# Kernel tuning notes

Measured on AMD Instinct MI355X. Metric: run time of the kernel, lower is better.

Reference implementation:

```python
import jax, jax.numpy as jnp
import numpy as np

N, E, D, L, G = 100000, 300000, 256, 5, 4096


def _bn(x, p):
    # p: [4, dim] = (gamma, beta, running_mean, running_var); eval-mode BatchNorm1d
    g, b, m, v = p
    return (x - m) * jax.lax.rsqrt(v + 1e-5) * g + b


def setup_inputs() -> dict:
    key = jax.random.key(0)
    ks = iter(jax.random.split(key, 48))

    def nrm(shape, scale=0.02):
        return jax.random.normal(next(ks), shape, dtype=jnp.float32) * scale

    def bn_params(n, dim):
        g = 1.0 + nrm((n, dim), 0.1)
        b = nrm((n, dim), 0.1)
        m = nrm((n, dim), 0.1)
        v = 1.0 + jax.random.uniform(next(ks), (n, dim), dtype=jnp.float32)
        return jnp.stack([g, b, m, v], axis=1)  # [n,4,dim]

    return {
        "x": jax.random.randint(next(ks), (N, 9), 0, 2, dtype=jnp.int32),
        "edge_index": jax.random.randint(next(ks), (2, E), 0, N, dtype=jnp.int32),
        "edge_attr": jax.random.randint(next(ks), (E, 3), 0, 2, dtype=jnp.int32),
        "batch": jnp.sort(jax.random.randint(next(ks), (N,), 0, G, dtype=jnp.int32)),
        "atom_emb": nrm((9, 120, D)),            # AtomEncoder: 9 feature tables
        "bond_emb": nrm((L, 3, 6, D)),           # per-layer BondEncoder: 3 feature tables
        "vn0": jnp.zeros((D,), jnp.float32),     # virtualnode embedding (init 0)
        "eps": jnp.zeros((L,), jnp.float32),     # GIN eps per layer
        "conv_W1": nrm((L, D, 2 * D), 1.0 / np.sqrt(D)),     # GIN MLP (sampled BayesLinear)
        "conv_b1": nrm((L, 2 * D)),
        "conv_bn1": bn_params(L, 2 * D),
        "conv_W2": nrm((L, 2 * D, D), 1.0 / np.sqrt(2 * D)),
        "conv_b2": nrm((L, D)),
        "node_bn": bn_params(L, D),              # per-layer outer BatchNorm
        "vn_W1": nrm((L - 1, D, D), 1.0 / np.sqrt(D)),       # virtual-node MLP
        "vn_b1": nrm((L - 1, D)),
        "vn_bn1": bn_params(L - 1, D),
        "vn_W2": nrm((L - 1, D, D), 1.0 / np.sqrt(D)),
        "vn_b2": nrm((L - 1, D)),
        "vn_bn2": bn_params(L - 1, D),
    }


def reference(x, edge_index, edge_attr, batch, atom_emb, bond_emb, vn0, eps,
              conv_W1, conv_b1, conv_bn1, conv_W2, conv_b2, node_bn,
              vn_W1, vn_b1, vn_bn1, vn_W2, vn_b2, vn_bn2):
    src, dst = edge_index[0], edge_index[1]
    n_nodes = x.shape[0]
    n_layers = conv_W1.shape[0]
    # AtomEncoder: sum of 9 feature embeddings -> [N, D]
    h = atom_emb[jnp.arange(9), x].sum(axis=1)
    vn = jnp.broadcast_to(vn0, (G, vn0.shape[0]))  # [G, D]
    for l in range(n_layers):
        # broadcast virtual node into graph's nodes
        h = h + vn[batch]
        # GINConv: msg = relu(x_j + bond_emb), sum-aggregate, MLP((1+eps)x + aggr)
        e = bond_emb[l][jnp.arange(3), edge_attr].sum(axis=1)  # [E, D]
        msg = jax.nn.relu(h[src] + e)
        aggr = jax.ops.segment_sum(msg, dst, num_segments=n_nodes)
        t = (1.0 + eps[l]) * h + aggr
        t = jax.nn.relu(_bn(t @ conv_W1[l] + conv_b1[l], conv_bn1[l])) @ conv_W2[l] + conv_b2[l]
        hn = _bn(t, node_bn[l])  # outer BatchNorm (eval); dropout is identity in eval
        if l < n_layers - 1:
            hn = jax.nn.relu(hn)
            # global_add_pool of pre-conv h, then virtual-node MLP update
            vtemp = jax.ops.segment_sum(h, batch, num_segments=G) + vn
            u = jax.nn.relu(_bn(vtemp @ vn_W1[l] + vn_b1[l], vn_bn1[l]))
            vn = jax.nn.relu(_bn(u @ vn_W2[l] + vn_b2[l], vn_bn2[l]))
        h = hn
    return h  # JK == 'last'
```

## Files before the change

kernel.cpp:

```cpp
#include <hip/hip_runtime.h>

#define NN 100000
#define EE 300000
#define DD 256
#define LL 5
#define GG 4096
#define DB 512
#define MPAD 100096

typedef __attribute__((ext_vector_type(4))) float f32x4;
typedef __attribute__((ext_vector_type(8))) short s16x8;

__device__ __forceinline__ ushort f2bf(float f) {
  unsigned u = __float_as_uint(f);
  return (ushort)((u + 0x7fffu + ((u >> 16) & 1u)) >> 16);
}
__device__ __forceinline__ float b2f(ushort u) {
  return __uint_as_float(((unsigned)u) << 16);
}

__device__ __forceinline__ void gload16(const void* g, void* l) {
  __builtin_amdgcn_global_load_lds((const __attribute__((address_space(1))) void*)g,
                                   (__attribute__((address_space(3))) void*)l, 16, 0, 0);
}

__global__ void k_atom(const int* __restrict__ x, const float* __restrict__ emb,
                       const float* __restrict__ vn0, ushort* __restrict__ hvb) {
  int n = blockIdx.x * 4 + (threadIdx.x >> 6);
  if (n >= NN) return;
  int d = (threadIdx.x & 63) * 4;
  const float4 v0 = *(const float4*)&vn0[d];
  float ax = v0.x, ay = v0.y, az = v0.z, aw = v0.w;
#pragma unroll
  for (int f = 0; f < 9; ++f) {
    int v = x[n * 9 + f];
    const float4 t = *(const float4*)&emb[((size_t)(f * 120 + v)) * DD + d];
    ax += t.x; ay += t.y; az += t.z; aw += t.w;
  }
  ushort4 o; o.x = f2bf(ax); o.y = f2bf(ay); o.z = f2bf(az); o.w = f2bf(aw);
  *(ushort4*)&hvb[(size_t)n * DD + d] = o;
}

__global__ void k_vninit(const float* __restrict__ vn0, float* __restrict__ vn) {
  int i = blockIdx.x * blockDim.x + threadIdx.x;
  if (i < GG * DD) vn[i] = vn0[i & (DD - 1)];
}

__global__ void k_goff(const int* __restrict__ batch, int* __restrict__ goff) {
  int g = blockIdx.x * blockDim.x + threadIdx.x;
  if (g > GG) return;
  if (g == GG) { goff[GG] = NN; return; }
  int lo = 0, hi = NN;
  while (lo < hi) { int mid = (lo + hi) >> 1; if (batch[mid] < g) lo = mid + 1; else hi = mid; }
  goff[g] = lo;
}

__global__ void k_zero(int* __restrict__ p, int n) {
  int i = blockIdx.x * 256 + threadIdx.x;
  if (i < n) p[i] = 0;
}

__global__ void k_deg(const int* __restrict__ dst, int* __restrict__ deg) {
  int e = blockIdx.x * 256 + threadIdx.x;
  if (e < EE) atomicAdd(&deg[dst[e]], 1);
}

__global__ void k_scan1(const int* __restrict__ deg, int* __restrict__ coff,
                        int* __restrict__ bsum) {
  __shared__ int wsum[16];
  __shared__ int wpre[16];
  int lane = threadIdx.x & 63, wid = threadIdx.x >> 6;
  int i = blockIdx.x * 1024 + threadIdx.x;
  int v = (i < NN) ? deg[i] : 0;
  int xv = v;
#pragma unroll
  for (int off = 1; off < 64; off <<= 1) {
    int y = __shfl_up(xv, off);
    if (lane >= off) xv += y;
  }
  if (lane == 63) wsum[wid] = xv;
  __syncthreads();
  if (wid == 0 && lane < 16) {
    int s = wsum[lane];
    int xx = s;
#pragma unroll
    for (int off = 1; off < 16; off <<= 1) {
      int y = __shfl_up(xx, off);
      if (lane >= off) xx += y;
    }
    wpre[lane] = xx - s;
  }
  __syncthreads();
  int val = xv + wpre[wid];
  if (i < NN) coff[i + 1] = val;
  if (threadIdx.x == 1023) bsum[blockIdx.x] = val;
}

__global__ void k_scan2(int* __restrict__ bsum, int nb) {
  __shared__ int ws[2];
  int t = threadIdx.x, lane = t & 63, wid = t >> 6;
  int v = (t < nb) ? bsum[t] : 0;
  int xv = v;
#pragma unroll
  for (int off = 1; off < 64; off <<= 1) {
    int y = __shfl_up(xv, off);
    if (lane >= off) xv += y;
  }
  if (lane == 63) ws[wid] = xv;
  __syncthreads();
  int incl = xv + ((wid == 1) ? ws[0] : 0);
  if (t < nb) bsum[t] = incl - v;
}

__global__ void k_scan3(int* __restrict__ coff, const int* __restrict__ bpre) {
  int i = blockIdx.x * 1024 + threadIdx.x;
  if (i == 0) coff[0] = 0;
  if (i < NN) coff[i + 1] += bpre[i >> 10];
}

__global__ void k_eposinit(const int* __restrict__ coff, int* __restrict__ epos) {
  int n = blockIdx.x * 256 + threadIdx.x;
  if (n < NN) epos[n] = coff[n];
}

__global__ void k_scatter(const int* __restrict__ dst, int* __restrict__ epos,
                          int* __restrict__ eid) {
  int e = blockIdx.x * 256 + threadIdx.x;
  if (e < EE) { int p = atomicAdd(&epos[dst[e]], 1); eid[p] = e; }
}

__global__ void k_sort(const int* __restrict__ coff, int* __restrict__ eid) {
  int n = blockIdx.x * 256 + threadIdx.x;
  if (n >= NN) return;
  int s = coff[n], t = coff[n + 1];
  for (int i = s + 1; i < t; ++i) {
    int key = eid[i]; int j = i - 1;
    while (j >= s && eid[j] > key) { eid[j + 1] = eid[j]; --j; }
    eid[j + 1] = key;
  }
}

__global__ void k_emeta(const int* __restrict__ eid, const int* __restrict__ srcs,
                        const int* __restrict__ eattr, unsigned* __restrict__ emeta) {
  int idx = blockIdx.x * 256 + threadIdx.x;
  if (idx >= EE) return;
  int e = eid[idx];
  int s = srcs[e];
  unsigned c = (unsigned)(eattr[e * 3 + 0] + 2 * eattr[e * 3 + 1] + 4 * eattr[e * 3 + 2]);
  emeta[idx] = (unsigned)s | (c << 17);
}

__global__ void k_bond8(const float* __restrict__ bondE, float* __restrict__ bond8) {
  int l = blockIdx.x, c = blockIdx.y, d = threadIdx.x;
  float v = bondE[(((size_t)l * 3 + 0) * 6 + (c & 1)) * DD + d]
          + bondE[(((size_t)l * 3 + 1) * 6 + ((c >> 1) & 1)) * DD + d]
          + bondE[(((size_t)l * 3 + 2) * 6 + ((c >> 2) & 1)) * DD + d];
  bond8[((size_t)l * 8 + c) * DD + d] = v;
}

__global__ void k_wt(const float* __restrict__ in, ushort* __restrict__ out, int K, int N) {
  __shared__ float t[16][17];
  int l = blockIdx.z;
  int kb = blockIdx.x * 16, nb = blockIdx.y * 16;
  int tx = threadIdx.x & 15, ty = threadIdx.x >> 4;
  t[ty][tx] = in[(size_t)l * K * N + (size_t)(kb + ty) * N + nb + tx];
  __syncthreads();
  out[(size_t)l * N * K + (size_t)(nb + ty) * K + kb + tx] = f2bf(t[tx][ty]);
}

__global__ void k_pool(const ushort* __restrict__ hvb, const float* __restrict__ vn,
                       ushort* __restrict__ vtempb, const int* __restrict__ goff) {
  int g = blockIdx.x * 4 + (threadIdx.x >> 6);
  if (g >= GG) return;
  int d = (threadIdx.x & 63) * 4;
  float4 v = *(const float4*)&vn[(size_t)g * DD + d];
  float ax = v.x, ay = v.y, az = v.z, aw = v.w;
  int r0 = goff[g], r1 = goff[g + 1];
  for (int r = r0; r < r1; ++r) {
    ushort4 hu = *(const ushort4*)&hvb[(size_t)r * DD + d];
    ax += b2f(hu.x); ay += b2f(hu.y); az += b2f(hu.z); aw += b2f(hu.w);
  }
  ushort4 o; o.x = f2bf(ax); o.y = f2bf(ay); o.z = f2bf(az); o.w = f2bf(aw);
  *(ushort4*)&vtempb[(size_t)g * DD + d] = o;
}

__global__ void k_aggr(const ushort* __restrict__ hvb, ushort* __restrict__ tb,
                       const unsigned* __restrict__ emeta, const int* __restrict__ coff,
                       const float* __restrict__ bond8l, const float* __restrict__ epsp,
                       int l) {
  int n = blockIdx.x * 4 + (threadIdx.x >> 6);
  if (n >= NN) return;
  int d = (threadIdx.x & 63) * 4;
  float ax = 0.f, ay = 0.f, az = 0.f, aw = 0.f;
  int s0 = coff[n], s1 = coff[n + 1];
  int idx = s0;
  for (; idx + 2 <= s1; idx += 2) {
    unsigned m0 = emeta[idx], m1 = emeta[idx + 1];
    const ushort4 h0 = *(const ushort4*)&hvb[(size_t)(m0 & 0x1FFFFu) * DD + d];
    const ushort4 h1 = *(const ushort4*)&hvb[(size_t)(m1 & 0x1FFFFu) * DD + d];
    const float4 b0 = *(const float4*)&bond8l[(size_t)(m0 >> 17) * DD + d];
    const float4 b1 = *(const float4*)&bond8l[(size_t)(m1 >> 17) * DD + d];
    ax += fmaxf(b2f(h0.x) + b0.x, 0.f) + fmaxf(b2f(h1.x) + b1.x, 0.f);
    ay += fmaxf(b2f(h0.y) + b0.y, 0.f) + fmaxf(b2f(h1.y) + b1.y, 0.f);
    az += fmaxf(b2f(h0.z) + b0.z, 0.f) + fmaxf(b2f(h1.z) + b1.z, 0.f);
    aw += fmaxf(b2f(h0.w) + b0.w, 0.f) + fmaxf(b2f(h1.w) + b1.w, 0.f);
  }
  if (idx < s1) {
    unsigned m0 = emeta[idx];
    const ushort4 h0 = *(const ushort4*)&hvb[(size_t)(m0 & 0x1FFFFu) * DD + d];
    const float4 b0 = *(const float4*)&bond8l[(size_t)(m0 >> 17) * DD + d];
    ax += fmaxf(b2f(h0.x) + b0.x, 0.f);
    ay += fmaxf(b2f(h0.y) + b0.y, 0.f);
    az += fmaxf(b2f(h0.z) + b0.z, 0.f);
    aw += fmaxf(b2f(h0.w) + b0.w, 0.f);
  }
  float ep = 1.f + epsp[l];
  const ushort4 hn = *(const ushort4*)&hvb[(size_t)n * DD + d];
  ushort4 o;
  o.x = f2bf(ep * b2f(hn.x) + ax); o.y = f2bf(ep * b2f(hn.y) + ay);
  o.z = f2bf(ep * b2f(hn.z) + az); o.w = f2bf(ep * b2f(hn.w) + aw);
  *(ushort4*)&tb[(size_t)n * DD + d] = o;
}

template<int K1, int N1, int N2>
__global__ __launch_bounds__(256) void k_mlp(
    const ushort* __restrict__ A, int M,
    const ushort* __restrict__ W1T, const ushort* __restrict__ W2T,
    const float* __restrict__ b1, const float* __restrict__ bn1,
    const float* __restrict__ b2, const float* __restrict__ bn2,
    void* __restrict__ Cv, int outBf16, int relu2,
    const float* __restrict__ vnAdd, const int* __restrict__ batchv) {
  constexpr int K2 = N1;
  constexpr int TM = 64;
  __shared__ ushort Wst[2][128 * 32];
  __shared__ ushort c1s[TM * N1];
  const int tid = threadIdx.x;
  const int lane = tid & 63;
  const int wv = tid >> 6;
  const int wr = wv >> 1, wc = wv & 1;
  const int r16 = lane & 15, kgrp = lane >> 4;
  const int rowBase = blockIdx.x * TM;

  const int ca0 = tid, ca1 = tid + 256;
  const int sc0 = ca0 >> 2, sk0 = (ca0 & 3) ^ ((sc0 >> 1) & 3);
  const int sc1 = ca1 >> 2, sk1 = (ca1 & 3) ^ ((sc1 >> 1) & 3);

  int boff[4];
#pragma unroll
  for (int n = 0; n < 4; ++n) {
    int cl = wc * 64 + n * 16 + r16;
    boff[n] = cl * 64 + ((kgrp ^ ((cl >> 1) & 3)) << 4);
  }

  const ushort* arow[2];
#pragma unroll
  for (int m = 0; m < 2; ++m)
    arow[m] = A + (size_t)(rowBase + wr * 32 + m * 16 + r16) * K1 + kgrp * 8;

  int arow2[2], ax7[2];
#pragma unroll
  for (int m = 0; m < 2; ++m) {
    int rl = wr * 32 + m * 16 + r16;
    arow2[m] = rl * (N1 * 2);
    ax7[m] = rl & 7;
  }

  f32x4 acc[2][4];

  for (int cc = 0; cc < N1 / 128; ++cc) {
    const ushort* Wc = W1T + (size_t)cc * 128 * K1;
    gload16(Wc + (size_t)sc0 * K1 + sk0 * 8, (char*)Wst[0] + ca0 * 16);
    gload16(Wc + (size_t)sc1 * K1 + sk1 * 8, (char*)Wst[0] + ca1 * 16);
#pragma unroll
    for (int m = 0; m < 2; ++m)
#pragma unroll
      for (int n = 0; n < 4; ++n) acc[m][n] = (f32x4)0.f;
    __syncthreads();
    int cur = 0;
    for (int t = 0; t < K1 / 32; ++t) {
      if (t + 1 < K1 / 32) {
        gload16(Wc + (size_t)sc0 * K1 + (t + 1) * 32 + sk0 * 8, (char*)Wst[cur ^ 1] + ca0 * 16);
        gload16(Wc + (size_t)sc1 * K1 + (t + 1) * 32 + sk1 * 8, (char*)Wst[cur ^ 1] + ca1 * 16);
      }
      s16x8 a[2], b[4];
#pragma unroll
      for (int m = 0; m < 2; ++m) a[m] = *(const s16x8*)(arow[m] + t * 32);
#pragma unroll
      for (int n = 0; n < 4; ++n) b[n] = *(const s16x8*)((const char*)Wst[cur] + boff[n]);
#pragma unroll
      for (int m = 0; m < 2; ++m)
#pragma unroll
        for (int n = 0; n < 4; ++n)
          acc[m][n] = __builtin_amdgcn_mfma_f32_16x16x32_bf16(a[m], b[n], acc[m][n], 0, 0, 0);
      __syncthreads();
      cur ^= 1;
    }
    float al[4], be[4];
#pragma unroll
    for (int n = 0; n < 4; ++n) {
      int col = cc * 128 + wc * 64 + n * 16 + r16;
      float g = bn1[col], bb = bn1[N1 + col], mm = bn1[2 * N1 + col], vv = bn1[3 * N1 + col];
      float s = g * rsqrtf(vv + 1e-5f);
      al[n] = s; be[n] = fmaf(b1[col] - mm, s, bb);
    }
#pragma unroll
    for (int m = 0; m < 2; ++m) {
#pragma unroll
      for (int r = 0; r < 4; ++r) {
        int rl = wr * 32 + m * 16 + kgrp * 4 + r;
        char* rowp = (char*)c1s + rl * (N1 * 2);
        int x7 = rl & 7;
#pragma unroll
        for (int n = 0; n < 4; ++n) {
          int col = cc * 128 + wc * 64 + n * 16 + r16;
          float v = fmaxf(fmaf(acc[m][n][r], al[n], be[n]), 0.f);
          int slot = (col >> 3) ^ x7;
          *(ushort*)(rowp + slot * 16 + (col & 7) * 2) = f2bf(v);
        }
      }
    }
  }

  for (int c2 = 0; c2 < N2 / 128; ++c2) {
    const ushort* Wc = W2T + (size_t)c2 * 128 * K2;
    gload16(Wc + (size_t)sc0 * K2 + sk0 * 8, (char*)Wst[0] + ca0 * 16);
    gload16(Wc + (size_t)sc1 * K2 + sk1 * 8, (char*)Wst[0] + ca1 * 16);
#pragma unroll
    for (int m = 0; m < 2; ++m)
#pragma unroll
      for (int n = 0; n < 4; ++n) acc[m][n] = (f32x4)0.f;
    __syncthreads();
    int cur = 0;
    for (int t = 0; t < K2 / 32; ++t) {
      if (t + 1 < K2 / 32) {
        gload16(Wc + (size_t)sc0 * K2 + (t + 1) * 32 + sk0 * 8, (char*)Wst[cur ^ 1] + ca0 * 16);
        gload16(Wc + (size_t)sc1 * K2 + (t + 1) * 32 + sk1 * 8, (char*)Wst[cur ^ 1] + ca1 * 16);
      }
      s16x8 a[2], b[4];
#pragma unroll
      for (int m = 0; m < 2; ++m)
        a[m] = *(const s16x8*)((const char*)c1s + arow2[m] + (((t * 4 + kgrp) ^ ax7[m]) << 4));
#pragma unroll
      for (int n = 0; n < 4; ++n) b[n] = *(const s16x8*)((const char*)Wst[cur] + boff[n]);
#pragma unroll
      for (int m = 0; m < 2; ++m)
#pragma unroll
        for (int n = 0; n < 4; ++n)
          acc[m][n] = __builtin_amdgcn_mfma_f32_16x16x32_bf16(a[m], b[n], acc[m][n], 0, 0, 0);
      __syncthreads();
      cur ^= 1;
    }
    float al[4], be[4];
#pragma unroll
    for (int n = 0; n < 4; ++n) {
      int col = c2 * 128 + wc * 64 + n * 16 + r16;
      float g = bn2[col], bb = bn2[N2 + col], mm = bn2[2 * N2 + col], vv = bn2[3 * N2 + col];
      float s = g * rsqrtf(vv + 1e-5f);
      al[n] = s; be[n] = fmaf(b2[col] - mm, s, bb);
    }
#pragma unroll
    for (int m = 0; m < 2; ++m) {
#pragma unroll
      for (int r = 0; r < 4; ++r) {
        int row = rowBase + wr * 32 + m * 16 + kgrp * 4 + r;
        if (row < M) {
          const float* vp = vnAdd ? (vnAdd + (size_t)batchv[row] * N2) : nullptr;
#pragma unroll
          for (int n = 0; n < 4; ++n) {
            int col = c2 * 128 + wc * 64 + n * 16 + r16;
            float v = fmaf(acc[m][n][r], al[n], be[n]);
            if (relu2) v = fmaxf(v, 0.f);
            if (vp) v += vp[col];
            if (outBf16) ((ushort*)Cv)[(size_t)row * N2 + col] = f2bf(v);
            else         ((float*)Cv)[(size_t)row * N2 + col] = v;
          }
        }
      }
    }
  }
}

extern "C" void kernel_launch(void* const* d_in, const int* in_sizes, int n_in,
                              void* d_out, int out_size, void* d_ws, size_t ws_size,
                              hipStream_t stream) {
  const int*   x     = (const int*)d_in[0];
  const int*   ei    = (const int*)d_in[1];
  const int*   ea    = (const int*)d_in[2];
  const int*   batch = (const int*)d_in[3];
  const float* atomE = (const float*)d_in[4];
  const float* bondE = (const float*)d_in[5];
  const float* vn0   = (const float*)d_in[6];
  const float* eps   = (const float*)d_in[7];
  const float* cW1   = (const float*)d_in[8];
  const float* cb1   = (const float*)d_in[9];
  const float* cbn1  = (const float*)d_in[10];
  const float* cW2   = (const float*)d_in[11];
  const float* cb2   = (const float*)d_in[12];
  const float* nbn   = (const float*)d_in[13];
  const float* vW1   = (const float*)d_in[14];
  const float* vb1   = (const float*)d_in[15];
  const float* vbn1  = (const float*)d_in[16];
  const float* vW2   = (const float*)d_in[17];
  const float* vb2   = (const float*)d_in[18];
  const float* vbn2  = (const float*)d_in[19];
  (void)in_sizes; (void)n_in; (void)out_size; (void)ws_size;

  char* wsp = (char*)d_ws;
  size_t o = 0;
  auto alloc = [&](size_t bytes) -> char* {
    char* p = wsp + o; o += (bytes + 255) & ~(size_t)255; return p;
  };
  ushort* tbuf  = (ushort*)alloc((size_t)MPAD * DD * 2);
  float*  vn    = (float*) alloc((size_t)GG * DD * 4);
  ushort* vtmpb = (ushort*)alloc((size_t)GG * DD * 2);
  ushort* bw1   = (ushort*)alloc((size_t)LL * DB * DD * 2);
  ushort* bw2   = (ushort*)alloc((size_t)LL * DD * DB * 2);
  ushort* bvw1  = (ushort*)alloc((size_t)(LL - 1) * DD * DD * 2);
  ushort* bvw2  = (ushort*)alloc((size_t)(LL - 1) * DD * DD * 2);
  float*  bond8 = (float*) alloc((size_t)LL * 8 * DD * 4);
  unsigned* emeta = (unsigned*)alloc((size_t)EE * 4);
  int* coff = (int*)alloc((size_t)(NN + 1) * 4);
  int* deg  = (int*)alloc((size_t)NN * 4);
  int* epos = (int*)alloc((size_t)NN * 4);
  int* eid  = (int*)alloc((size_t)EE * 4);
  int* goff = (int*)alloc((size_t)(GG + 1) * 4);
  int* bsum = (int*)alloc((size_t)128 * 4);

  const int* srcs = ei;
  const int* dsts = ei + EE;
  ushort* hvb = (ushort*)d_out;

  k_atom<<<(NN + 3) / 4, 256, 0, stream>>>(x, atomE, vn0, hvb);
  k_vninit<<<(GG * DD + 255) / 256, 256, 0, stream>>>(vn0, vn);
  k_goff<<<(GG + 256) / 256, 256, 0, stream>>>(batch, goff);
  k_zero<<<(NN + 255) / 256, 256, 0, stream>>>(deg, NN);
  k_deg<<<(EE + 255) / 256, 256, 0, stream>>>(dsts, deg);
  {
    int nb = (NN + 1023) / 1024;
    k_scan1<<<nb, 1024, 0, stream>>>(deg, coff, bsum);
    k_scan2<<<1, 128, 0, stream>>>(bsum, nb);
    k_scan3<<<nb, 1024, 0, stream>>>(coff, bsum);
  }
  k_eposinit<<<(NN + 255) / 256, 256, 0, stream>>>(coff, epos);
  k_scatter<<<(EE + 255) / 256, 256, 0, stream>>>(dsts, epos, eid);
  k_sort<<<(NN + 255) / 256, 256, 0, stream>>>(coff, eid);
  k_emeta<<<(EE + 255) / 256, 256, 0, stream>>>(eid, srcs, ea, emeta);
  k_bond8<<<dim3(LL, 8), 256, 0, stream>>>(bondE, bond8);
  k_wt<<<dim3(DD / 16, DB / 16, LL), 256, 0, stream>>>(cW1, bw1, DD, DB);
  k_wt<<<dim3(DB / 16, DD / 16, LL), 256, 0, stream>>>(cW2, bw2, DB, DD);
  k_wt<<<dim3(DD / 16, DD / 16, LL - 1), 256, 0, stream>>>(vW1, bvw1, DD, DD);
  k_wt<<<dim3(DD / 16, DD / 16, LL - 1), 256, 0, stream>>>(vW2, bvw2, DD, DD);

  for (int l = 0; l < LL; ++l) {
    if (l < LL - 1) {
      k_pool<<<(GG + 3) / 4, 256, 0, stream>>>(hvb, vn, vtmpb, goff);
      k_mlp<256, 256, 256><<<GG / 64, 256, 0, stream>>>(
          vtmpb, GG, bvw1 + (size_t)l * DD * DD, bvw2 + (size_t)l * DD * DD,
          vb1 + (size_t)l * DD, vbn1 + (size_t)l * 4 * DD,
          vb2 + (size_t)l * DD, vbn2 + (size_t)l * 4 * DD,
          vn, 0, 1, nullptr, nullptr);
    }
    k_aggr<<<(NN + 3) / 4, 256, 0, stream>>>(hvb, tbuf, emeta, coff,
                                             bond8 + (size_t)l * 8 * DD, eps, l);
    if (l < LL - 1) {
      k_mlp<256, 512, 256><<<MPAD / 64, 256, 0, stream>>>(
          tbuf, NN, bw1 + (size_t)l * DB * DD, bw2 + (size_t)l * DD * DB,
          cb1 + (size_t)l * DB, cbn1 + (size_t)l * 4 * DB,
          cb2 + (size_t)l * DD, nbn + (size_t)l * 4 * DD,
          hvb, 1, 1, vn, batch);
    } else {
      k_mlp<256, 512, 256><<<MPAD / 64, 256, 0, stream>>>(
          tbuf, NN, bw1 + (size_t)l * DB * DD, bw2 + (size_t)l * DD * DB,
          cb1 + (size_t)l * DB, cbn1 + (size_t)l * 4 * DB,
          cb2 + (size_t)l * DD, nbn + (size_t)l * 4 * DD,
          (float*)d_out, 0, 0, nullptr, nullptr);
    }
  }
}
```

Baseline: 1.257 ms.

## Split fused node MLP into two tiled MFMA GEMMs with bf16 intermediate

Replaces the fused two-layer node MLP kernel, which kept the 512-wide intermediate in shared memory per 64-row tile, with two separate 128x128-tile MFMA GEMM launches that go through a bf16 intermediate buffer in global memory. The first GEMM uses an XCD-aware block remap so that consecutive tiles land on the same die for better L2 reuse of A. The aim is larger tiles, more A/B reuse per block and better occupancy than the fused kernel, at the cost of writing and re-reading a 100k x 512 bf16 intermediate and one extra launch per layer.

```diff
diff --git a/kernel.cpp b/kernel.cpp
--- a/kernel.cpp
+++ b/kernel.cpp
@@ -222,14 +222,124 @@
   *(ushort4*)&tb[(size_t)n * DD + d] = o;
 }
 
+__global__ __launch_bounds__(256) void k_mfma_gemm(
+    const ushort* __restrict__ A, int M, int K,
+    const ushort* __restrict__ BT, int N, int CT, int remap,
+    void* __restrict__ Cv, int outBf16, int doRelu,
+    const float* __restrict__ bias, const float* __restrict__ bn,
+    const float* __restrict__ vnAdd, const int* __restrict__ batchv) {
+  __shared__ ushort Asm[2][128 * 32];
+  __shared__ ushort Bsm[2][128 * 32];
+  int rowBase, colBase;
+  if (remap) {
+    const int T = gridDim.x;
+    const int q = T >> 3, r = T & 7;
+    const int xcd = blockIdx.x & 7, li = blockIdx.x >> 3;
+    const int w0 = xcd * q + (xcd < r ? xcd : r) + li;
+    rowBase = (w0 / CT) * 128;
+    colBase = (w0 % CT) * 128;
+  } else {
+    rowBase = blockIdx.x * 128;
+    colBase = blockIdx.y * 128;
+  }
+  const int tid = threadIdx.x;
+  const int lane = tid & 63;
+  const int wv = tid >> 6;
+  const int wrow = (wv >> 1) * 64, wcol = (wv & 1) * 64;
+  const int r16 = lane & 15, kgrp = lane >> 4;
+
+  f32x4 acc[4][4];
+#pragma unroll
+  for (int m = 0; m < 4; ++m)
+#pragma unroll
+    for (int n = 0; n < 4; ++n) acc[m][n] = (f32x4)0.f;
+
+  const int ca0 = tid, ca1 = tid + 256;
+  const int ra0 = ca0 >> 2, ka0 = (ca0 & 3) ^ ((ra0 >> 1) & 3);
+  const int ra1 = ca1 >> 2, ka1 = (ca1 & 3) ^ ((ra1 >> 1) & 3);
+  const ushort* Ap0 = A + (size_t)(rowBase + ra0) * K + ka0 * 8;
+  const ushort* Ap1 = A + (size_t)(rowBase + ra1) * K + ka1 * 8;
+  const ushort* Bp0 = BT + (size_t)(colBase + ra0) * K + ka0 * 8;
+  const ushort* Bp1 = BT + (size_t)(colBase + ra1) * K + ka1 * 8;
+
+  int aoff[4], boff[4];
+#pragma unroll
+  for (int m = 0; m < 4; ++m) {
+    int row = wrow + m * 16 + r16;
+    aoff[m] = row * 64 + ((kgrp ^ ((row >> 1) & 3)) << 4);
+    int col = wcol + m * 16 + r16;
+    boff[m] = col * 64 + ((kgrp ^ ((col >> 1) & 3)) << 4);
+  }
+
+  const int nk = K >> 5;
+  gload16(Ap0, (char*)Asm + ca0 * 16);
+  gload16(Ap1, (char*)Asm + ca1 * 16);
+  gload16(Bp0, (char*)Bsm + ca0 * 16);
+  gload16(Bp1, (char*)Bsm + ca1 * 16);
+  __syncthreads();
+
+  int cur = 0;
+  for (int t = 0; t < nk; ++t) {
+    int nxt = cur ^ 1;
+    if (t + 1 < nk) {
+      int ko = (t + 1) << 5;
+      gload16(Ap0 + ko, (char*)Asm + nxt * 8192 + ca0 * 16);
+      gload16(Ap1 + ko, (char*)Asm + nxt * 8192 + ca1 * 16);
+      gload16(Bp0 + ko, (char*)Bsm + nxt * 8192 + ca0 * 16);
+      gload16(Bp1 + ko, (char*)Bsm + nxt * 8192 + ca1 * 16);
+    }
+    const char* cA = (const char*)Asm + cur * 8192;
+    const char* cB = (const char*)Bsm + cur * 8192;
+    s16x8 a[4], b[4];
+#pragma unroll
+    for (int m = 0; m < 4; ++m) a[m] = *(const s16x8*)(cA + aoff[m]);
+#pragma unroll
+    for (int n = 0; n < 4; ++n) b[n] = *(const s16x8*)(cB + boff[n]);
+#pragma unroll
+    for (int m = 0; m < 4; ++m)
+#pragma unroll
+      for (int n = 0; n < 4; ++n)
+        acc[m][n] = __builtin_amdgcn_mfma_f32_16x16x32_bf16(a[m], b[n], acc[m][n], 0, 0, 0);
+    __syncthreads();
+    cur = nxt;
+  }
+
+  float alpha[4], beta[4];
+#pragma unroll
+  for (int n = 0; n < 4; ++n) {
+    int col = colBase + wcol + n * 16 + r16;
+    float g = bn[col], bb = bn[N + col], mm = bn[2 * N + col], vv = bn[3 * N + col];
+    float s = g * rsqrtf(vv + 1e-5f);
+    alpha[n] = s; beta[n] = fmaf(bias[col] - mm, s, bb);
+  }
+#pragma unroll
+  for (int m = 0; m < 4; ++m) {
+#pragma unroll
+    for (int rr = 0; rr < 4; ++rr) {
+      int row = rowBase + wrow + m * 16 + kgrp * 4 + rr;
+      if (row < M) {
+        const float* vp = vnAdd ? (vnAdd + (size_t)batchv[row] * N) : nullptr;
+#pragma unroll
+        for (int n = 0; n < 4; ++n) {
+          int col = colBase + wcol + n * 16 + r16;
+          float v = fmaf(acc[m][n][rr], alpha[n], beta[n]);
+          if (doRelu) v = fmaxf(v, 0.f);
+          if (vp) v += vp[col];
+          if (outBf16) ((ushort*)Cv)[(size_t)row * N + col] = f2bf(v);
+          else         ((float*)Cv)[(size_t)row * N + col] = v;
+        }
+      }
+    }
+  }
+}
+
 template<int K1, int N1, int N2>
 __global__ __launch_bounds__(256) void k_mlp(
     const ushort* __restrict__ A, int M,
     const ushort* __restrict__ W1T, const ushort* __restrict__ W2T,
     const float* __restrict__ b1, const float* __restrict__ bn1,
     const float* __restrict__ b2, const float* __restrict__ bn2,
-    void* __restrict__ Cv, int outBf16, int relu2,
-    const float* __restrict__ vnAdd, const int* __restrict__ batchv) {
+    void* __restrict__ Cv, int outBf16, int relu2) {
   constexpr int K2 = N1;
   constexpr int TM = 64;
   __shared__ ushort Wst[2][128 * 32];
@@ -364,13 +474,11 @@
       for (int r = 0; r < 4; ++r) {
         int row = rowBase + wr * 32 + m * 16 + kgrp * 4 + r;
         if (row < M) {
-          const float* vp = vnAdd ? (vnAdd + (size_t)batchv[row] * N2) : nullptr;
 #pragma unroll
           for (int n = 0; n < 4; ++n) {
             int col = c2 * 128 + wc * 64 + n * 16 + r16;
             float v = fmaf(acc[m][n][r], al[n], be[n]);
             if (relu2) v = fmaxf(v, 0.f);
-            if (vp) v += vp[col];
             if (outBf16) ((ushort*)Cv)[(size_t)row * N2 + col] = f2bf(v);
             else         ((float*)Cv)[(size_t)row * N2 + col] = v;
           }
@@ -411,6 +519,7 @@
     char* p = wsp + o; o += (bytes + 255) & ~(size_t)255; return p;
   };
   ushort* tbuf  = (ushort*)alloc((size_t)MPAD * DD * 2);
+  ushort* c1b   = (ushort*)alloc((size_t)MPAD * DB * 2);
   float*  vn    = (float*) alloc((size_t)GG * DD * 4);
   ushort* vtmpb = (ushort*)alloc((size_t)GG * DD * 2);
   ushort* bw1   = (ushort*)alloc((size_t)LL * DB * DD * 2);
@@ -458,22 +567,22 @@
           vtmpb, GG, bvw1 + (size_t)l * DD * DD, bvw2 + (size_t)l * DD * DD,
           vb1 + (size_t)l * DD, vbn1 + (size_t)l * 4 * DD,
           vb2 + (size_t)l * DD, vbn2 + (size_t)l * 4 * DD,
-          vn, 0, 1, nullptr, nullptr);
+          vn, 0, 1);
     }
     k_aggr<<<(NN + 3) / 4, 256, 0, stream>>>(hvb, tbuf, emeta, coff,
                                              bond8 + (size_t)l * 8 * DD, eps, l);
+    k_mfma_gemm<<<(MPAD / 128) * 4, 256, 0, stream>>>(
+        tbuf, NN, DD, bw1 + (size_t)l * DB * DD, DB, 4, 1,
+        c1b, 1, 1, cb1 + (size_t)l * DB, cbn1 + (size_t)l * 4 * DB, nullptr, nullptr);
     if (l < LL - 1) {
-      k_mlp<256, 512, 256><<<MPAD / 64, 256, 0, stream>>>(
-          tbuf, NN, bw1 + (size_t)l * DB * DD, bw2 + (size_t)l * DD * DB,
-          cb1 + (size_t)l * DB, cbn1 + (size_t)l * 4 * DB,
-          cb2 + (size_t)l * DD, nbn + (size_t)l * 4 * DD,
-          hvb, 1, 1, vn, batch);
+      k_mfma_gemm<<<dim3(MPAD / 128, DD / 128), 256, 0, stream>>>(
+          c1b, NN, DB, bw2 + (size_t)l * DD * DB, DD, 0, 0,
+          hvb, 1, 1, cb2 + (size_t)l * DD, nbn + (size_t)l * 4 * DD, vn, batch);
     } else {
-      k_mlp<256, 512, 256><<<MPAD / 64, 256, 0, stream>>>(
-          tbuf, NN, bw1 + (size_t)l * DB * DD, bw2 + (size_t)l * DD * DB,
-          cb1 + (size_t)l * DB, cbn1 + (size_t)l * 4 * DB,
-          cb2 + (size_t)l * DD, nbn + (size_t)l * 4 * DD,
-          (float*)d_out, 0, 0, nullptr, nullptr);
-    }
-  }
-}
+      k_mfma_gemm<<<dim3(MPAD / 128, DD / 128), 256, 0, stream>>>(
+          c1b, NN, DB, bw2 + (size_t)l * DD * DB, DD, 0, 0,
+          (float*)d_out, 0, 0, cb2 + (size_t)l * DD, nbn + (size_t)l * 4 * DD,
+          nullptr, nullptr);
+    }
+  }
+}
```

After: 1.194 ms. 5.0% less time.
